# Kernel optimization log

Hardware: AMD Instinct MI355X
Metric: run time of the kernel (lower is better)

Reference implementation:

```python
import jax, jax.numpy as jnp
import numpy as np
import math

D = 768
SCALE = math.sqrt(D)


def setup_inputs() -> dict:
    key = jax.random.key(0)
    k1, k2, k3, k4 = jax.random.split(key, 4)
    lhs = jax.random.normal(k1, (8, 1024, D), dtype=jnp.float32)
    rhs = jax.random.normal(k2, (8, 1024, D), dtype=jnp.float32)
    # xavier_normal_ std = sqrt(2/(fan_in+fan_out))
    std = math.sqrt(2.0 / (D + D))
    W_lhs = jax.random.normal(k3, (D, D), dtype=jnp.float32) * std
    W_rhs = jax.random.normal(k4, (D, D), dtype=jnp.float32) * std
    return {"lhs": lhs, "rhs": rhs, "W_lhs": W_lhs, "W_rhs": W_rhs}


def reference(lhs, rhs, W_lhs, W_rhs):
    # Linear (no bias): x @ W.T, then tanh
    l = jnp.tanh(jnp.einsum('nld,ed->nle', lhs, W_lhs))  # (N, L, D)
    r = jnp.tanh(jnp.einsum('nrd,ed->nre', rhs, W_rhs))  # (N, R, D)
    scores = jnp.einsum('nld,nrd->nlr', l, r)            # (N, L, R)
    attn_lhs = jax.nn.softmax(scores, axis=2)            # unscaled, row softmax
    attn_rhs = jax.nn.softmax(scores / SCALE, axis=1)    # scaled, column softmax
    out_lhs = jnp.einsum('nlr,nrd->nld', attn_lhs, rhs)
    out_rhs = jnp.einsum('nlr,nld->nrd', attn_rhs, lhs)
    return (jnp.concatenate([lhs, out_lhs], axis=2),
            jnp.concatenate([rhs, out_rhs], axis=2))
```

## Files before the change

kernel.cpp:

```cpp
#include <hip/hip_runtime.h>

typedef _Float16 f16_t;
typedef _Float16 f16x4 __attribute__((ext_vector_type(4)));
typedef _Float16 f16x8 __attribute__((ext_vector_type(8)));
typedef float floatx4 __attribute__((ext_vector_type(4)));

#define NB 8
#define SEQ 1024
#define DIM 768
#define INV_SCALE 0.03608439182435161f
#define ROW_SHIFT 40.0f

__device__ inline void async_load16(const void* g, void* l) {
  __builtin_amdgcn_global_load_lds((__attribute__((address_space(1))) void*)g,
                                   (__attribute__((address_space(3))) void*)l,
                                   16, 0, 0);
}


__global__ __launch_bounds__(256, 3) void gemm_proj(
    const f16_t* __restrict__ A0, const f16_t* __restrict__ W0,
    const f16_t* __restrict__ A1, const f16_t* __restrict__ W1,
    f16_t* __restrict__ C0, f16_t* __restrict__ C1) {
  __shared__ __align__(16) f16_t sA[128 * 64];
  __shared__ __align__(16) f16_t sB[128 * 64];
  const int b = blockIdx.x;
  const int xcd = b & 7, slot = b >> 3;
  const int grp = slot / 6, j = slot - grp * 6;
  const int stripe = grp * 8 + xcd;
  const int z = stripe >> 6, my = stripe & 63;
  const f16_t* Ab = (z ? A1 : A0) + (size_t)my * 128 * DIM;
  const f16_t* Bb = (z ? W1 : W0) + (size_t)j * 128 * DIM;
  f16_t* C = z ? C1 : C0;
  const int tid = threadIdx.x;
  const int lane = tid & 63;
  const int wave = tid >> 6;
  const int wr = wave >> 1, wc = wave & 1;
  const int fr = lane & 15;
  const int fq = lane >> 4;
  const int swz = ((lane & 7) ^ (lane >> 3)) << 3;
  const int x7 = (fr & 7) << 3;

  floatx4 acc[4][4] = {};

  for (int kt = 0; kt < DIM; kt += 64) {
    #pragma unroll
    for (int i = 0; i < 4; ++i) {
      const int ch = i * 4 + wave;
      const int row = ch * 8 + (lane >> 3);
      const size_t g = (size_t)row * DIM + kt + swz;
      async_load16(Ab + g, (char*)sA + ch * 1024);
      async_load16(Bb + g, (char*)sB + ch * 1024);
    }
    __syncthreads();
    #pragma unroll
    for (int ks = 0; ks < 64; ks += 32) {
      f16x8 af[4], bf[4];
      #pragma unroll
      for (int t = 0; t < 4; ++t) {
        const int cs = (ks + fq * 8) ^ x7;
        af[t] = *(const f16x8*)&sA[(wr * 64 + t * 16 + fr) * 64 + cs];
        bf[t] = *(const f16x8*)&sB[(wc * 64 + t * 16 + fr) * 64 + cs];
      }
      #pragma unroll
      for (int ti = 0; ti < 4; ++ti)
        #pragma unroll
        for (int tj = 0; tj < 4; ++tj)
          acc[ti][tj] = __builtin_amdgcn_mfma_f32_16x16x32_f16(
              af[ti], bf[tj], acc[ti][tj], 0, 0, 0);
    }
    __syncthreads();
  }

  const size_t m0 = (size_t)my * 128, n0 = (size_t)j * 128;
  #pragma unroll
  for (int ti = 0; ti < 4; ++ti)
    #pragma unroll
    for (int tj = 0; tj < 4; ++tj) {
      const size_t gm = m0 + wr * 64 + ti * 16 + fq * 4;
      const size_t gn = n0 + wc * 64 + tj * 16 + fr;
      #pragma unroll
      for (int i = 0; i < 4; ++i)
        C[(gm + i) * DIM + gn] = (f16_t)tanhf(acc[ti][tj][i]);
    }
}

__global__ __launch_bounds__(256, 3) void gemm_scores(
    const f16_t* __restrict__ A, const f16_t* __restrict__ B,
    float* __restrict__ C, float* __restrict__ rowpart,
    float* __restrict__ colpart) {
  __shared__ __align__(16) f16_t sA[128 * 64];
  __shared__ __align__(16) f16_t sB[128 * 64];
  const int b = blockIdx.x;
  const int xcd = b & 7, slot = b >> 3;
  const int grp = slot >> 3, j = slot & 7;
  const int stripe = grp * 8 + xcd;
  const int z = stripe >> 3, my = stripe & 7;
  const f16_t* Ab = A + (size_t)z * SEQ * DIM + (size_t)my * 128 * DIM;
  const f16_t* Bb = B + (size_t)z * SEQ * DIM + (size_t)j * 128 * DIM;
  const int tid = threadIdx.x;
  const int lane = tid & 63;
  const int wave = tid >> 6;
  const int wr = wave >> 1, wc = wave & 1;
  const int fr = lane & 15;
  const int fq = lane >> 4;
  const int swz = ((lane & 7) ^ (lane >> 3)) << 3;
  const int x7 = (fr & 7) << 3;

  floatx4 acc[4][4] = {};

  for (int kt = 0; kt < DIM; kt += 64) {
    #pragma unroll
    for (int i = 0; i < 4; ++i) {
      const int ch = i * 4 + wave;
      const int row = ch * 8 + (lane >> 3);
      const size_t g = (size_t)row * DIM + kt + swz;
      async_load16(Ab + g, (char*)sA + ch * 1024);
      async_load16(Bb + g, (char*)sB + ch * 1024);
    }
    __syncthreads();
    #pragma unroll
    for (int ks = 0; ks < 64; ks += 32) {
      f16x8 af[4], bf[4];
      #pragma unroll
      for (int t = 0; t < 4; ++t) {
        const int cs = (ks + fq * 8) ^ x7;
        af[t] = *(const f16x8*)&sA[(wr * 64 + t * 16 + fr) * 64 + cs];
        bf[t] = *(const f16x8*)&sB[(wc * 64 + t * 16 + fr) * 64 + cs];
      }
      #pragma unroll
      for (int ti = 0; ti < 4; ++ti)
        #pragma unroll
        for (int tj = 0; tj < 4; ++tj)
          acc[ti][tj] = __builtin_amdgcn_mfma_f32_16x16x32_f16(
              af[ti], bf[tj], acc[ti][tj], 0, 0, 0);
    }
    __syncthreads();
  }

  const size_t m0 = (size_t)my * 128, n0 = (size_t)j * 128;
  float* Cb = C + (size_t)z * SEQ * SEQ;
  #pragma unroll
  for (int ti = 0; ti < 4; ++ti)
    #pragma unroll
    for (int tj = 0; tj < 4; ++tj) {
      const size_t gm = m0 + wr * 64 + ti * 16 + fq * 4;
      const size_t gn = n0 + wc * 64 + tj * 16 + fr;
      #pragma unroll
      for (int i = 0; i < 4; ++i) Cb[(gm + i) * SEQ + gn] = acc[ti][tj][i];
    }

  float* srow = (float*)sA;
  float* scol = (float*)sB;
  #pragma unroll
  for (int ti = 0; ti < 4; ++ti)
    #pragma unroll
    for (int i = 0; i < 4; ++i) {
      float s = 0.f;
      #pragma unroll
      for (int tj = 0; tj < 4; ++tj) s += __expf(acc[ti][tj][i] - ROW_SHIFT);
      s += __shfl_xor(s, 1, 64);
      s += __shfl_xor(s, 2, 64);
      s += __shfl_xor(s, 4, 64);
      s += __shfl_xor(s, 8, 64);
      if (fr == 0) srow[wc * 128 + wr * 64 + ti * 16 + fq * 4 + i] = s;
    }
  #pragma unroll
  for (int tj = 0; tj < 4; ++tj) {
    float s = 0.f;
    #pragma unroll
    for (int ti = 0; ti < 4; ++ti)
      #pragma unroll
      for (int i = 0; i < 4; ++i) s += __expf(acc[ti][tj][i] * INV_SCALE);
    s += __shfl_xor(s, 16, 64);
    s += __shfl_xor(s, 32, 64);
    if (fq == 0) scol[wr * 128 + wc * 64 + tj * 16 + fr] = s;
  }
  __syncthreads();
  if (tid < 128)
    rowpart[((size_t)(z * 8 + j)) * SEQ + my * 128 + tid] =
        srow[tid] + srow[128 + tid];
  else
    colpart[((size_t)(z * 8 + my)) * SEQ + j * 128 + (tid - 128)] =
        scol[tid - 128] + scol[tid];
}

__global__ __launch_bounds__(256, 3) void gemm_apply(
    const f16_t* __restrict__ attn_l, const f16_t* __restrict__ attn_rT,
    const f16_t* __restrict__ rhsT, const f16_t* __restrict__ lhsT,
    float* __restrict__ out0, float* __restrict__ out1) {
  __shared__ __align__(16) f16_t sA[128 * 64];
  __shared__ __align__(16) f16_t sB[128 * 64];
  const int b = blockIdx.x;
  const int xcd = b & 7, slot = b >> 3;
  const int grp = slot / 6, j = slot - grp * 6;
  const int stripe = grp * 8 + xcd;
  const int z = stripe >> 3, my = stripe & 7;
  const int n = z & 7;
  const f16_t* Ab = (z < 8 ? attn_l : attn_rT) + (size_t)n * SEQ * SEQ +
                    (size_t)my * 128 * SEQ;
  const f16_t* Bb = (z < 8 ? rhsT : lhsT) + (size_t)n * SEQ * DIM +
                    (size_t)j * 128 * SEQ;
  float* C = (z < 8 ? out0 : out1) + (size_t)n * SEQ * 2 * DIM + DIM;
  const int tid = threadIdx.x;
  const int lane = tid & 63;
  const int wave = tid >> 6;
  const int wr = wave >> 1, wc = wave & 1;
  const int fr = lane & 15;
  const int fq = lane >> 4;
  const int swz = ((lane & 7) ^ (lane >> 3)) << 3;
  const int x7 = (fr & 7) << 3;

  floatx4 acc[4][4] = {};

  for (int kt = 0; kt < SEQ; kt += 64) {
    #pragma unroll
    for (int i = 0; i < 4; ++i) {
      const int ch = i * 4 + wave;
      const int row = ch * 8 + (lane >> 3);
      const size_t g = (size_t)row * SEQ + kt + swz;
      async_load16(Ab + g, (char*)sA + ch * 1024);
      async_load16(Bb + g, (char*)sB + ch * 1024);
    }
    __syncthreads();
    #pragma unroll
    for (int ks = 0; ks < 64; ks += 32) {
      f16x8 af[4], bf[4];
      #pragma unroll
      for (int t = 0; t < 4; ++t) {
        const int cs = (ks + fq * 8) ^ x7;
        af[t] = *(const f16x8*)&sA[(wr * 64 + t * 16 + fr) * 64 + cs];
        bf[t] = *(const f16x8*)&sB[(wc * 64 + t * 16 + fr) * 64 + cs];
      }
      #pragma unroll
      for (int ti = 0; ti < 4; ++ti)
        #pragma unroll
        for (int tj = 0; tj < 4; ++tj)
          acc[ti][tj] = __builtin_amdgcn_mfma_f32_16x16x32_f16(
              af[ti], bf[tj], acc[ti][tj], 0, 0, 0);
    }
    __syncthreads();
  }

  const size_t m0 = (size_t)my * 128, n0 = (size_t)j * 128;
  #pragma unroll
  for (int ti = 0; ti < 4; ++ti)
    #pragma unroll
    for (int tj = 0; tj < 4; ++tj) {
      const size_t gm = m0 + wr * 64 + ti * 16 + fq * 4;
      const size_t gn = n0 + wc * 64 + tj * 16 + fr;
      #pragma unroll
      for (int i = 0; i < 4; ++i)
        C[(gm + i) * (2 * DIM) + gn] = acc[ti][tj][i];
    }
}

__global__ __launch_bounds__(256) void cast_copy4(
    const float4* __restrict__ lhs, const float4* __restrict__ rhs,
    f16_t* __restrict__ lf, f16_t* __restrict__ rf, float4* __restrict__ o0,
    float4* __restrict__ o1) {
  const int which = blockIdx.y;
  const float4* in = which ? rhs : lhs;
  f16_t* out = which ? rf : lf;
  float4* outh = which ? o1 : o0;
  const int idx = blockIdx.x * 256 + threadIdx.x;
  const float4 v = in[idx];
  const int i4 = idx * 4;
  f16x4 h = {(f16_t)v.x, (f16_t)v.y, (f16_t)v.z, (f16_t)v.w};
  *(f16x4*)(out + i4) = h;
  const int row = i4 / DIM, col = i4 % DIM;
  outh[((size_t)row * (2 * DIM) + col) >> 2] = v;
}

__global__ __launch_bounds__(256) void castW(const float4* __restrict__ Wl,
                                             const float4* __restrict__ Wr,
                                             f16_t* __restrict__ ol,
                                             f16_t* __restrict__ orr) {
  const int which = blockIdx.y;
  const float4* in = which ? Wr : Wl;
  f16_t* out = which ? orr : ol;
  const int idx = blockIdx.x * 256 + threadIdx.x;
  const float4 v = in[idx];
  f16x4 h = {(f16_t)v.x, (f16_t)v.y, (f16_t)v.z, (f16_t)v.w};
  *(f16x4*)(out + idx * 4) = h;
}

__global__ __launch_bounds__(256) void transpose_cast(
    const float* __restrict__ lhs, const float* __restrict__ rhs,
    f16_t* __restrict__ lhsT, f16_t* __restrict__ rhsT) {
  __shared__ float tile[64][65];
  const int z = blockIdx.z;
  const int n = z & 7;
  const float* in = (z < 8 ? lhs : rhs) + (size_t)n * SEQ * DIM;
  f16_t* out = (z < 8 ? lhsT : rhsT) + (size_t)n * SEQ * DIM;
  const int c0 = blockIdx.x * 64, r0 = blockIdx.y * 64;
  const int x = threadIdx.x & 63, y = threadIdx.x >> 6;
  #pragma unroll
  for (int yy = y; yy < 64; yy += 4)
    tile[yy][x] = in[(size_t)(r0 + yy) * DIM + c0 + x];
  __syncthreads();
  #pragma unroll
  for (int yy = y; yy < 64; yy += 4)
    out[(size_t)(c0 + yy) * SEQ + r0 + x] = (f16_t)tile[x][yy];
}

__global__ __launch_bounds__(256) void finish_stats(
    const float* __restrict__ rowpart, const float* __restrict__ colpart,
    float* __restrict__ rowsum, float* __restrict__ colsum) {
  int t = blockIdx.x * 256 + threadIdx.x;
  const int side = t >> 13;
  t &= 8191;
  const int n = t >> 10, r = t & 1023;
  const float* part = side ? colpart : rowpart;
  float s = 0.f;
  #pragma unroll
  for (int k = 0; k < 8; ++k) s += part[((size_t)(n * 8 + k)) * SEQ + r];
  (side ? colsum : rowsum)[t] = s;
}

__global__ __launch_bounds__(256) void attn_write(
    const float* __restrict__ scores, const float* __restrict__ rowsum,
    const float* __restrict__ colsum, f16_t* __restrict__ attn_l,
    f16_t* __restrict__ attn_rT) {
  __shared__ float tile[64][65];
  const int n = blockIdx.z;
  const int c0 = blockIdx.x * 64, l0 = blockIdx.y * 64;
  const float* s = scores + (size_t)n * SEQ * SEQ;
  const int t = threadIdx.x;
  const int tr = t >> 4, tc4 = (t & 15) * 4;
  const float4 cs = *(const float4*)&colsum[n * SEQ + c0 + tc4];
  const float ci0 = 1.f / cs.x, ci1 = 1.f / cs.y, ci2 = 1.f / cs.z,
              ci3 = 1.f / cs.w;
  #pragma unroll
  for (int it = 0; it < 4; ++it) {
    const int row = tr + it * 16;
    const float4 v = *(const float4*)&s[(size_t)(l0 + row) * SEQ + c0 + tc4];
    const float rinv = 1.f / rowsum[n * SEQ + l0 + row];
    f16x4 al = {(f16_t)(__expf(v.x - ROW_SHIFT) * rinv),
                (f16_t)(__expf(v.y - ROW_SHIFT) * rinv),
                (f16_t)(__expf(v.z - ROW_SHIFT) * rinv),
                (f16_t)(__expf(v.w - ROW_SHIFT) * rinv)};
    *(f16x4*)&attn_l[(size_t)n * SEQ * SEQ + (size_t)(l0 + row) * SEQ + c0 +
                     tc4] = al;
    tile[row][tc4 + 0] = __expf(v.x * INV_SCALE) * ci0;
    tile[row][tc4 + 1] = __expf(v.y * INV_SCALE) * ci1;
    tile[row][tc4 + 2] = __expf(v.z * INV_SCALE) * ci2;
    tile[row][tc4 + 3] = __expf(v.w * INV_SCALE) * ci3;
  }
  __syncthreads();
  #pragma unroll
  for (int it = 0; it < 4; ++it) {
    const int cr = tr + it * 16;
    f16x4 o = {(f16_t)tile[tc4 + 0][cr], (f16_t)tile[tc4 + 1][cr],
               (f16_t)tile[tc4 + 2][cr], (f16_t)tile[tc4 + 3][cr]};
    *(f16x4*)&attn_rT[(size_t)n * SEQ * SEQ + (size_t)(c0 + cr) * SEQ + l0 +
                      tc4] = o;
  }
}

extern "C" void kernel_launch(void* const* d_in, const int* in_sizes, int n_in,
                              void* d_out, int out_size, void* d_ws,
                              size_t ws_size, hipStream_t stream) {
  const float* lhs = (const float*)d_in[0];
  const float* rhs = (const float*)d_in[1];
  const float* Wl = (const float*)d_in[2];
  const float* Wr = (const float*)d_in[3];
  float* out0 = (float*)d_out;
  float* out1 = out0 + (size_t)NB * SEQ * (2 * DIM);

  char* ws = (char*)d_ws;
  f16_t* lhs_f = (f16_t*)(ws + 0);
  f16_t* rhs_f = (f16_t*)(ws + 12582912);
  float* scores = (float*)(ws + 0);
  f16_t* l_f = (f16_t*)(ws + 33554432);
  f16_t* r_f = (f16_t*)(ws + 46137344);
  f16_t* Wl_h = (f16_t*)(ws + 58720256);
  f16_t* Wr_h = (f16_t*)(ws + 59899904);
  f16_t* attn_l = (f16_t*)(ws + 33554432);
  f16_t* attn_rT = (f16_t*)(ws + 50331648);
  f16_t* lhsT = (f16_t*)(ws + 67108864);
  f16_t* rhsT = (f16_t*)(ws + 79691776);
  float* rowsum = (float*)(ws + 92274688);
  float* colsum = (float*)(ws + 92307456);
  float* rowpart = (float*)(ws + 92340224);
  float* colpart = (float*)(ws + 92602368);

  cast_copy4<<<dim3(6144, 2), 256, 0, stream>>>((const float4*)lhs,
                                                (const float4*)rhs, lhs_f,
                                                rhs_f, (float4*)out0,
                                                (float4*)out1);
  castW<<<dim3(576, 2), 256, 0, stream>>>((const float4*)Wl, (const float4*)Wr,
                                          Wl_h, Wr_h);
  transpose_cast<<<dim3(12, 16, 16), 256, 0, stream>>>(lhs, rhs, lhsT, rhsT);
  gemm_proj<<<768, 256, 0, stream>>>(lhs_f, Wl_h, rhs_f, Wr_h, l_f, r_f);
  gemm_scores<<<512, 256, 0, stream>>>(l_f, r_f, scores, rowpart, colpart);
  finish_stats<<<64, 256, 0, stream>>>(rowpart, colpart, rowsum, colsum);
  attn_write<<<dim3(16, 16, NB), 256, 0, stream>>>(scores, rowsum, colsum,
                                                   attn_l, attn_rT);
  gemm_apply<<<768, 256, 0, stream>>>(attn_l, attn_rT, rhsT, lhsT, out0,
                                      out1);
}
```

Measured before the change: 270.7 us.

## Fuse softmax exp into scores GEMM and defer normalization to apply epilogue

The scores GEMM now writes unnormalized exponentials directly, as bf16 for the row softmax and as a transposed f16 array for the column softmax, instead of fp32 scores. This removes the fp32 score round trip and the finish_stats and attn_write kernels. The apply GEMM sums the partial denominators itself and scales its output rows by the reciprocal. The three cast and transpose kernels are merged into one prep kernel, and the row path switches to bf16 MFMA for range. The risks are lower precision, since bf16 carries unnormalized row exponentials, and uncoalesced scattered 2-byte and transposed stores in the scores epilogue.

```diff
diff --git a/kernel.cpp b/kernel.cpp
--- a/kernel.cpp
+++ b/kernel.cpp
@@ -3,6 +3,8 @@
 typedef _Float16 f16_t;
 typedef _Float16 f16x4 __attribute__((ext_vector_type(4)));
 typedef _Float16 f16x8 __attribute__((ext_vector_type(8)));
+typedef short s16x8 __attribute__((ext_vector_type(8)));
+typedef unsigned short u16x4 __attribute__((ext_vector_type(4)));
 typedef float floatx4 __attribute__((ext_vector_type(4)));
 
 #define NB 8
@@ -10,6 +12,12 @@
 #define DIM 768
 #define INV_SCALE 0.03608439182435161f
 #define ROW_SHIFT 40.0f
+
+__device__ inline unsigned short f2bf(float f) {
+  unsigned u = __builtin_bit_cast(unsigned, f);
+  u += 0x7fffu + ((u >> 16) & 1u);
+  return (unsigned short)(u >> 16);
+}
 
 __device__ inline void async_load16(const void* g, void* l) {
   __builtin_amdgcn_global_load_lds((__attribute__((address_space(1))) void*)g,
@@ -87,8 +95,8 @@
 
 __global__ __launch_bounds__(256, 3) void gemm_scores(
     const f16_t* __restrict__ A, const f16_t* __restrict__ B,
-    float* __restrict__ C, float* __restrict__ rowpart,
-    float* __restrict__ colpart) {
+    unsigned short* __restrict__ e_l, f16_t* __restrict__ e_rT,
+    float* __restrict__ rowpart, float* __restrict__ colpart) {
   __shared__ __align__(16) f16_t sA[128 * 64];
   __shared__ __align__(16) f16_t sB[128 * 64];
   const int b = blockIdx.x;
@@ -139,39 +147,45 @@
   }
 
   const size_t m0 = (size_t)my * 128, n0 = (size_t)j * 128;
-  float* Cb = C + (size_t)z * SEQ * SEQ;
-  #pragma unroll
-  for (int ti = 0; ti < 4; ++ti)
-    #pragma unroll
-    for (int tj = 0; tj < 4; ++tj) {
-      const size_t gm = m0 + wr * 64 + ti * 16 + fq * 4;
-      const size_t gn = n0 + wc * 64 + tj * 16 + fr;
-      #pragma unroll
-      for (int i = 0; i < 4; ++i) Cb[(gm + i) * SEQ + gn] = acc[ti][tj][i];
-    }
-
+  unsigned short* eL = e_l + (size_t)z * SEQ * SEQ;
+  f16_t* eT = e_rT + (size_t)z * SEQ * SEQ;
   float* srow = (float*)sA;
   float* scol = (float*)sB;
-  #pragma unroll
-  for (int ti = 0; ti < 4; ++ti)
+
+  #pragma unroll
+  for (int ti = 0; ti < 4; ++ti) {
     #pragma unroll
     for (int i = 0; i < 4; ++i) {
+      const size_t row = m0 + wr * 64 + ti * 16 + fq * 4 + i;
       float s = 0.f;
       #pragma unroll
-      for (int tj = 0; tj < 4; ++tj) s += __expf(acc[ti][tj][i] - ROW_SHIFT);
+      for (int tj = 0; tj < 4; ++tj) {
+        const float e = __expf(acc[ti][tj][i] - ROW_SHIFT);
+        s += e;
+        eL[row * SEQ + n0 + wc * 64 + tj * 16 + fr] = f2bf(e);
+      }
       s += __shfl_xor(s, 1, 64);
       s += __shfl_xor(s, 2, 64);
       s += __shfl_xor(s, 4, 64);
       s += __shfl_xor(s, 8, 64);
       if (fr == 0) srow[wc * 128 + wr * 64 + ti * 16 + fq * 4 + i] = s;
     }
+  }
   #pragma unroll
   for (int tj = 0; tj < 4; ++tj) {
+    const size_t coln = n0 + wc * 64 + tj * 16 + fr;
     float s = 0.f;
     #pragma unroll
-    for (int ti = 0; ti < 4; ++ti)
-      #pragma unroll
-      for (int i = 0; i < 4; ++i) s += __expf(acc[ti][tj][i] * INV_SCALE);
+    for (int ti = 0; ti < 4; ++ti) {
+      f16x4 ev;
+      #pragma unroll
+      for (int i = 0; i < 4; ++i) {
+        const float e = __expf(acc[ti][tj][i] * INV_SCALE);
+        s += e;
+        ev[i] = (f16_t)e;
+      }
+      *(f16x4*)&eT[coln * SEQ + m0 + wr * 64 + ti * 16 + fq * 4] = ev;
+    }
     s += __shfl_xor(s, 16, 64);
     s += __shfl_xor(s, 32, 64);
     if (fq == 0) scol[wr * 128 + wc * 64 + tj * 16 + fr] = s;
@@ -185,23 +199,11 @@
         scol[tid - 128] + scol[tid];
 }
 
-__global__ __launch_bounds__(256, 3) void gemm_apply(
-    const f16_t* __restrict__ attn_l, const f16_t* __restrict__ attn_rT,
-    const f16_t* __restrict__ rhsT, const f16_t* __restrict__ lhsT,
-    float* __restrict__ out0, float* __restrict__ out1) {
-  __shared__ __align__(16) f16_t sA[128 * 64];
-  __shared__ __align__(16) f16_t sB[128 * 64];
-  const int b = blockIdx.x;
-  const int xcd = b & 7, slot = b >> 3;
-  const int grp = slot / 6, j = slot - grp * 6;
-  const int stripe = grp * 8 + xcd;
-  const int z = stripe >> 3, my = stripe & 7;
-  const int n = z & 7;
-  const f16_t* Ab = (z < 8 ? attn_l : attn_rT) + (size_t)n * SEQ * SEQ +
-                    (size_t)my * 128 * SEQ;
-  const f16_t* Bb = (z < 8 ? rhsT : lhsT) + (size_t)n * SEQ * DIM +
-                    (size_t)j * 128 * SEQ;
-  float* C = (z < 8 ? out0 : out1) + (size_t)n * SEQ * 2 * DIM + DIM;
+template <bool BF>
+__device__ __forceinline__ void apply_body(
+    const f16_t* __restrict__ Ab, const f16_t* __restrict__ Bb,
+    float* __restrict__ C, const float* __restrict__ pp, f16_t* sA, f16_t* sB,
+    float* sinv) {
   const int tid = threadIdx.x;
   const int lane = tid & 63;
   const int wave = tid >> 6;
@@ -211,6 +213,13 @@
   const int swz = ((lane & 7) ^ (lane >> 3)) << 3;
   const int x7 = (fr & 7) << 3;
 
+  if (tid < 128) {
+    float s = 0.f;
+    #pragma unroll
+    for (int k = 0; k < 8; ++k) s += pp[k * SEQ + tid];
+    sinv[tid] = 1.f / s;
+  }
+
   floatx4 acc[4][4] = {};
 
   for (int kt = 0; kt < SEQ; kt += 64) {
@@ -225,136 +234,127 @@
     __syncthreads();
     #pragma unroll
     for (int ks = 0; ks < 64; ks += 32) {
-      f16x8 af[4], bf[4];
-      #pragma unroll
-      for (int t = 0; t < 4; ++t) {
-        const int cs = (ks + fq * 8) ^ x7;
-        af[t] = *(const f16x8*)&sA[(wr * 64 + t * 16 + fr) * 64 + cs];
-        bf[t] = *(const f16x8*)&sB[(wc * 64 + t * 16 + fr) * 64 + cs];
-      }
-      #pragma unroll
-      for (int ti = 0; ti < 4; ++ti)
+      const int cs = (ks + fq * 8) ^ x7;
+      #pragma unroll
+      for (int ti = 0; ti < 4; ++ti) {
+        const f16_t* pa = &sA[(wr * 64 + ti * 16 + fr) * 64 + cs];
         #pragma unroll
-        for (int tj = 0; tj < 4; ++tj)
-          acc[ti][tj] = __builtin_amdgcn_mfma_f32_16x16x32_f16(
-              af[ti], bf[tj], acc[ti][tj], 0, 0, 0);
-    }
-    __syncthreads();
-  }
-
+        for (int tj = 0; tj < 4; ++tj) {
+          const f16_t* pb = &sB[(wc * 64 + tj * 16 + fr) * 64 + cs];
+          if constexpr (BF)
+            acc[ti][tj] = __builtin_amdgcn_mfma_f32_16x16x32_bf16(
+                *(const s16x8*)pa, *(const s16x8*)pb, acc[ti][tj], 0, 0, 0);
+          else
+            acc[ti][tj] = __builtin_amdgcn_mfma_f32_16x16x32_f16(
+                *(const f16x8*)pa, *(const f16x8*)pb, acc[ti][tj], 0, 0, 0);
+        }
+      }
+    }
+    __syncthreads();
+  }
+
+  #pragma unroll
+  for (int ti = 0; ti < 4; ++ti) {
+    const int gm = wr * 64 + ti * 16 + fq * 4;
+    const floatx4 iv = *(const floatx4*)&sinv[gm];
+    #pragma unroll
+    for (int tj = 0; tj < 4; ++tj) {
+      const int gn = wc * 64 + tj * 16 + fr;
+      #pragma unroll
+      for (int i = 0; i < 4; ++i)
+        C[(size_t)(gm + i) * (2 * DIM) + gn] = acc[ti][tj][i] * iv[i];
+    }
+  }
+}
+
+__global__ __launch_bounds__(256, 3) void gemm_apply(
+    const f16_t* __restrict__ e_l, const f16_t* __restrict__ e_rT,
+    const f16_t* __restrict__ rhsT, const f16_t* __restrict__ lhsT,
+    const float* __restrict__ rowpart, const float* __restrict__ colpart,
+    float* __restrict__ out0, float* __restrict__ out1) {
+  __shared__ __align__(16) f16_t sA[128 * 64];
+  __shared__ __align__(16) f16_t sB[128 * 64];
+  __shared__ __align__(16) float sinv[128];
+  const int b = blockIdx.x;
+  const int xcd = b & 7, slot = b >> 3;
+  const int grp = slot / 6, j = slot - grp * 6;
+  const int stripe = grp * 8 + xcd;
+  const int z = stripe >> 3, my = stripe & 7;
+  const int n = z & 7;
   const size_t m0 = (size_t)my * 128, n0 = (size_t)j * 128;
-  #pragma unroll
-  for (int ti = 0; ti < 4; ++ti)
-    #pragma unroll
-    for (int tj = 0; tj < 4; ++tj) {
-      const size_t gm = m0 + wr * 64 + ti * 16 + fq * 4;
-      const size_t gn = n0 + wc * 64 + tj * 16 + fr;
-      #pragma unroll
-      for (int i = 0; i < 4; ++i)
-        C[(gm + i) * (2 * DIM) + gn] = acc[ti][tj][i];
-    }
-}
-
-__global__ __launch_bounds__(256) void cast_copy4(
-    const float4* __restrict__ lhs, const float4* __restrict__ rhs,
-    f16_t* __restrict__ lf, f16_t* __restrict__ rf, float4* __restrict__ o0,
-    float4* __restrict__ o1) {
-  const int which = blockIdx.y;
-  const float4* in = which ? rhs : lhs;
-  f16_t* out = which ? rf : lf;
-  float4* outh = which ? o1 : o0;
-  const int idx = blockIdx.x * 256 + threadIdx.x;
-  const float4 v = in[idx];
-  const int i4 = idx * 4;
-  f16x4 h = {(f16_t)v.x, (f16_t)v.y, (f16_t)v.z, (f16_t)v.w};
-  *(f16x4*)(out + i4) = h;
-  const int row = i4 / DIM, col = i4 % DIM;
-  outh[((size_t)row * (2 * DIM) + col) >> 2] = v;
-}
-
-__global__ __launch_bounds__(256) void castW(const float4* __restrict__ Wl,
-                                             const float4* __restrict__ Wr,
-                                             f16_t* __restrict__ ol,
-                                             f16_t* __restrict__ orr) {
-  const int which = blockIdx.y;
-  const float4* in = which ? Wr : Wl;
-  f16_t* out = which ? orr : ol;
-  const int idx = blockIdx.x * 256 + threadIdx.x;
-  const float4 v = in[idx];
-  f16x4 h = {(f16_t)v.x, (f16_t)v.y, (f16_t)v.z, (f16_t)v.w};
-  *(f16x4*)(out + idx * 4) = h;
-}
-
-__global__ __launch_bounds__(256) void transpose_cast(
+  if (z < 8) {
+    apply_body<true>(e_l + (size_t)n * SEQ * SEQ + m0 * SEQ,
+                     rhsT + (size_t)n * SEQ * DIM + n0 * SEQ,
+                     out0 + (size_t)n * SEQ * 2 * DIM + DIM + m0 * 2 * DIM + n0,
+                     rowpart + (size_t)n * 8 * SEQ + m0, sA, sB, sinv);
+  } else {
+    apply_body<false>(
+        e_rT + (size_t)n * SEQ * SEQ + m0 * SEQ,
+        lhsT + (size_t)n * SEQ * DIM + n0 * SEQ,
+        out1 + (size_t)n * SEQ * 2 * DIM + DIM + m0 * 2 * DIM + n0,
+        colpart + (size_t)n * 8 * SEQ + m0, sA, sB, sinv);
+  }
+}
+
+__global__ __launch_bounds__(256) void prep(
     const float* __restrict__ lhs, const float* __restrict__ rhs,
-    f16_t* __restrict__ lhsT, f16_t* __restrict__ rhsT) {
+    const float* __restrict__ Wl, const float* __restrict__ Wr,
+    f16_t* __restrict__ lf, f16_t* __restrict__ rf, f16_t* __restrict__ lhsT,
+    unsigned short* __restrict__ rhsT, f16_t* __restrict__ Wlh,
+    f16_t* __restrict__ Wrh, float* __restrict__ o0, float* __restrict__ o1) {
+  const int z = blockIdx.z;
+  const int tid = threadIdx.x;
+  const int x4 = (tid & 15) * 4, ty = tid >> 4;
+  const int c0 = blockIdx.x * 64, r0 = blockIdx.y * 64;
+  if (z >= 16) {
+    if (blockIdx.y >= 12) return;
+    const float* in = (z == 17 ? Wr : Wl);
+    f16_t* out = (z == 17 ? Wrh : Wlh);
+    #pragma unroll
+    for (int it = 0; it < 4; ++it) {
+      const int row = r0 + ty + it * 16;
+      const float4 v = *(const float4*)&in[(size_t)row * DIM + c0 + x4];
+      f16x4 h = {(f16_t)v.x, (f16_t)v.y, (f16_t)v.z, (f16_t)v.w};
+      *(f16x4*)&out[(size_t)row * DIM + c0 + x4] = h;
+    }
+    return;
+  }
   __shared__ float tile[64][65];
-  const int z = blockIdx.z;
   const int n = z & 7;
   const float* in = (z < 8 ? lhs : rhs) + (size_t)n * SEQ * DIM;
-  f16_t* out = (z < 8 ? lhsT : rhsT) + (size_t)n * SEQ * DIM;
-  const int c0 = blockIdx.x * 64, r0 = blockIdx.y * 64;
-  const int x = threadIdx.x & 63, y = threadIdx.x >> 6;
-  #pragma unroll
-  for (int yy = y; yy < 64; yy += 4)
-    tile[yy][x] = in[(size_t)(r0 + yy) * DIM + c0 + x];
+  f16_t* fout = (z < 8 ? lf : rf) + (size_t)n * SEQ * DIM;
+  float* oh = (z < 8 ? o0 : o1) + (size_t)n * SEQ * 2 * DIM;
+  #pragma unroll
+  for (int it = 0; it < 4; ++it) {
+    const int row = ty + it * 16;
+    const float4 v = *(const float4*)&in[(size_t)(r0 + row) * DIM + c0 + x4];
+    f16x4 h = {(f16_t)v.x, (f16_t)v.y, (f16_t)v.z, (f16_t)v.w};
+    *(f16x4*)&fout[(size_t)(r0 + row) * DIM + c0 + x4] = h;
+    *(float4*)&oh[(size_t)(r0 + row) * 2 * DIM + c0 + x4] = v;
+    tile[row][x4 + 0] = v.x;
+    tile[row][x4 + 1] = v.y;
+    tile[row][x4 + 2] = v.z;
+    tile[row][x4 + 3] = v.w;
+  }
   __syncthreads();
-  #pragma unroll
-  for (int yy = y; yy < 64; yy += 4)
-    out[(size_t)(c0 + yy) * SEQ + r0 + x] = (f16_t)tile[x][yy];
-}
-
-__global__ __launch_bounds__(256) void finish_stats(
-    const float* __restrict__ rowpart, const float* __restrict__ colpart,
-    float* __restrict__ rowsum, float* __restrict__ colsum) {
-  int t = blockIdx.x * 256 + threadIdx.x;
-  const int side = t >> 13;
-  t &= 8191;
-  const int n = t >> 10, r = t & 1023;
-  const float* part = side ? colpart : rowpart;
-  float s = 0.f;
-  #pragma unroll
-  for (int k = 0; k < 8; ++k) s += part[((size_t)(n * 8 + k)) * SEQ + r];
-  (side ? colsum : rowsum)[t] = s;
-}
-
-__global__ __launch_bounds__(256) void attn_write(
-    const float* __restrict__ scores, const float* __restrict__ rowsum,
-    const float* __restrict__ colsum, f16_t* __restrict__ attn_l,
-    f16_t* __restrict__ attn_rT) {
-  __shared__ float tile[64][65];
-  const int n = blockIdx.z;
-  const int c0 = blockIdx.x * 64, l0 = blockIdx.y * 64;
-  const float* s = scores + (size_t)n * SEQ * SEQ;
-  const int t = threadIdx.x;
-  const int tr = t >> 4, tc4 = (t & 15) * 4;
-  const float4 cs = *(const float4*)&colsum[n * SEQ + c0 + tc4];
-  const float ci0 = 1.f / cs.x, ci1 = 1.f / cs.y, ci2 = 1.f / cs.z,
-              ci3 = 1.f / cs.w;
-  #pragma unroll
-  for (int it = 0; it < 4; ++it) {
-    const int row = tr + it * 16;
-    const float4 v = *(const float4*)&s[(size_t)(l0 + row) * SEQ + c0 + tc4];
-    const float rinv = 1.f / rowsum[n * SEQ + l0 + row];
-    f16x4 al = {(f16_t)(__expf(v.x - ROW_SHIFT) * rinv),
-                (f16_t)(__expf(v.y - ROW_SHIFT) * rinv),
-                (f16_t)(__expf(v.z - ROW_SHIFT) * rinv),
-                (f16_t)(__expf(v.w - ROW_SHIFT) * rinv)};
-    *(f16x4*)&attn_l[(size_t)n * SEQ * SEQ + (size_t)(l0 + row) * SEQ + c0 +
-                     tc4] = al;
-    tile[row][tc4 + 0] = __expf(v.x * INV_SCALE) * ci0;
-    tile[row][tc4 + 1] = __expf(v.y * INV_SCALE) * ci1;
-    tile[row][tc4 + 2] = __expf(v.z * INV_SCALE) * ci2;
-    tile[row][tc4 + 3] = __expf(v.w * INV_SCALE) * ci3;
-  }
-  __syncthreads();
-  #pragma unroll
-  for (int it = 0; it < 4; ++it) {
-    const int cr = tr + it * 16;
-    f16x4 o = {(f16_t)tile[tc4 + 0][cr], (f16_t)tile[tc4 + 1][cr],
-               (f16_t)tile[tc4 + 2][cr], (f16_t)tile[tc4 + 3][cr]};
-    *(f16x4*)&attn_rT[(size_t)n * SEQ * SEQ + (size_t)(c0 + cr) * SEQ + l0 +
-                      tc4] = o;
+  if (z < 8) {
+    f16_t* T = lhsT + (size_t)n * SEQ * DIM;
+    #pragma unroll
+    for (int it = 0; it < 4; ++it) {
+      const int cr = ty + it * 16;
+      f16x4 o = {(f16_t)tile[x4 + 0][cr], (f16_t)tile[x4 + 1][cr],
+                 (f16_t)tile[x4 + 2][cr], (f16_t)tile[x4 + 3][cr]};
+      *(f16x4*)&T[(size_t)(c0 + cr) * SEQ + r0 + x4] = o;
+    }
+  } else {
+    unsigned short* T = rhsT + (size_t)n * SEQ * DIM;
+    #pragma unroll
+    for (int it = 0; it < 4; ++it) {
+      const int cr = ty + it * 16;
+      u16x4 o = {f2bf(tile[x4 + 0][cr]), f2bf(tile[x4 + 1][cr]),
+                 f2bf(tile[x4 + 2][cr]), f2bf(tile[x4 + 3][cr])};
+      *(u16x4*)&T[(size_t)(c0 + cr) * SEQ + r0 + x4] = o;
+    }
   }
 }
 
@@ -369,34 +369,25 @@
   float* out1 = out0 + (size_t)NB * SEQ * (2 * DIM);
 
   char* ws = (char*)d_ws;
-  f16_t* lhs_f = (f16_t*)(ws + 0);
-  f16_t* rhs_f = (f16_t*)(ws + 12582912);
-  float* scores = (float*)(ws + 0);
-  f16_t* l_f = (f16_t*)(ws + 33554432);
-  f16_t* r_f = (f16_t*)(ws + 46137344);
-  f16_t* Wl_h = (f16_t*)(ws + 58720256);
-  f16_t* Wr_h = (f16_t*)(ws + 59899904);
-  f16_t* attn_l = (f16_t*)(ws + 33554432);
-  f16_t* attn_rT = (f16_t*)(ws + 50331648);
-  f16_t* lhsT = (f16_t*)(ws + 67108864);
-  f16_t* rhsT = (f16_t*)(ws + 79691776);
-  float* rowsum = (float*)(ws + 92274688);
-  float* colsum = (float*)(ws + 92307456);
-  float* rowpart = (float*)(ws + 92340224);
-  float* colpart = (float*)(ws + 92602368);
-
-  cast_copy4<<<dim3(6144, 2), 256, 0, stream>>>((const float4*)lhs,
-                                                (const float4*)rhs, lhs_f,
-                                                rhs_f, (float4*)out0,
-                                                (float4*)out1);
-  castW<<<dim3(576, 2), 256, 0, stream>>>((const float4*)Wl, (const float4*)Wr,
-                                          Wl_h, Wr_h);
-  transpose_cast<<<dim3(12, 16, 16), 256, 0, stream>>>(lhs, rhs, lhsT, rhsT);
+  f16_t* lhsT = (f16_t*)(ws + 0);
+  unsigned short* rhsT = (unsigned short*)(ws + 12582912);
+  f16_t* l_f = (f16_t*)(ws + 25165824);
+  f16_t* r_f = (f16_t*)(ws + 37748736);
+  f16_t* lhs_f = (f16_t*)(ws + 50331648);
+  f16_t* rhs_f = (f16_t*)(ws + 62914560);
+  f16_t* Wl_h = (f16_t*)(ws + 75497472);
+  f16_t* Wr_h = (f16_t*)(ws + 76677120);
+  unsigned short* e_l = (unsigned short*)(ws + 50331648);
+  f16_t* e_rT = (f16_t*)(ws + 67108864);
+  float* rowpart = (float*)(ws + 83886080);
+  float* colpart = (float*)(ws + 84148224);
+
+  prep<<<dim3(12, 16, 18), 256, 0, stream>>>(lhs, rhs, Wl, Wr, lhs_f, rhs_f,
+                                             lhsT, rhsT, Wl_h, Wr_h, out0,
+                                             out1);
   gemm_proj<<<768, 256, 0, stream>>>(lhs_f, Wl_h, rhs_f, Wr_h, l_f, r_f);
-  gemm_scores<<<512, 256, 0, stream>>>(l_f, r_f, scores, rowpart, colpart);
-  finish_stats<<<64, 256, 0, stream>>>(rowpart, colpart, rowsum, colsum);
-  attn_write<<<dim3(16, 16, NB), 256, 0, stream>>>(scores, rowsum, colsum,
-                                                   attn_l, attn_rT);
-  gemm_apply<<<768, 256, 0, stream>>>(attn_l, attn_rT, rhsT, lhsT, out0,
-                                      out1);
-}
+  gemm_scores<<<512, 256, 0, stream>>>(l_f, r_f, e_l, e_rT, rowpart, colpart);
+  gemm_apply<<<768, 256, 0, stream>>>((const f16_t*)e_l, e_rT,
+                                      (const f16_t*)rhsT, lhsT, rowpart,
+                                      colpart, out0, out1);
+}
```

Result: faster. 251.3 us (-7.2%).
